# Performance work log

Measured on AMD Instinct MI355X. Metric: run time of the kernel, lower is better.

## Reference

```python
import jax, jax.numpy as jnp
import numpy as np

K = 3  # kernel_size=(3,3), flat all-ones structuring element


def _erode(x):
    # flat erosion = sliding-window min, SAME padding with +inf (geodesic)
    return jax.lax.reduce_window(x, float('inf'), jax.lax.min,
                                 (1, 1, K, K), (1, 1, 1, 1), 'SAME')


def _dilate(x):
    # flat dilation = sliding-window max, SAME padding with -inf
    return jax.lax.reduce_window(x, -float('inf'), jax.lax.max,
                                 (1, 1, K, K), (1, 1, 1, 1), 'SAME')


def setup_inputs() -> dict:
    key = jax.random.key(0)
    x = jax.random.uniform(key, (16, 3, 1024, 1024), dtype=jnp.float32)
    return {"x": x}


def reference(x) -> jnp.ndarray:
    # morphological opening: dilation(erosion(x)) with flat 3x3 SE,
    # applied per-channel (kernel repeated over channels in the original)
    return _dilate(_erode(x))
```

## Files before the change

kernel.cpp:

```cpp
#include <hip/hip_runtime.h>


#define IMG_H 1024
#define IMG_W 1024
#define TX 128
#define TY 16
#define IN_W (TX + 8)
#define IN_H (TY + 4)
#define ER_W (TX + 2)
#define ER_H (TY + 2)
#define NT 256

__global__ __launch_bounds__(NT)
void open3x3_fused(const float* __restrict__ in, float* __restrict__ out) {
    __shared__ float s_in[IN_H][IN_W];
    __shared__ float s_h [IN_H][ER_W];
    __shared__ float s_e [ER_H][ER_W];
    __shared__ float s_m [ER_H][TX];

    const int t  = threadIdx.x;
    const int ox = blockIdx.x * TX;
    const int oy = blockIdx.y * TY;
    const int img_elems = IMG_H * IMG_W;
    const float* img  = in  + (size_t)blockIdx.z * img_elems;
    float*       outp = out + (size_t)blockIdx.z * img_elems;

    const float PINF = __builtin_inff();
    const float NINF = -__builtin_inff();

    for (int idx = t; idx < IN_H * (IN_W / 4); idx += NT) {
        int row = idx / (IN_W / 4);
        int c4  = idx % (IN_W / 4);
        int r = oy - 2 + row;
        int c = ox - 4 + 4 * c4;
        float4 v;
        if (r >= 0 && r < IMG_H && c >= 0 && c + 3 < IMG_W) {
            v = *(const float4*)(img + r * IMG_W + c);
        } else {
            const float* rowp = img + r * IMG_W;
            bool rin = (r >= 0 && r < IMG_H);
            v.x = (rin && c + 0 >= 0 && c + 0 < IMG_W) ? rowp[c + 0] : PINF;
            v.y = (rin && c + 1 >= 0 && c + 1 < IMG_W) ? rowp[c + 1] : PINF;
            v.z = (rin && c + 2 >= 0 && c + 2 < IMG_W) ? rowp[c + 2] : PINF;
            v.w = (rin && c + 3 >= 0 && c + 3 < IMG_W) ? rowp[c + 3] : PINF;
        }
        *(float4*)&s_in[row][4 * c4] = v;
    }
    __syncthreads();

    for (int idx = t; idx < IN_H * ER_W; idx += NT) {
        int y = idx / ER_W;
        int x = idx % ER_W;
        int sx = x + 3;
        float a = s_in[y][sx - 1];
        float b = s_in[y][sx];
        float c = s_in[y][sx + 1];
        s_h[y][x] = fminf(fminf(a, b), c);
    }
    __syncthreads();

    for (int idx = t; idx < ER_H * ER_W; idx += NT) {
        int y = idx / ER_W;
        int x = idx % ER_W;
        int r = oy - 1 + y;
        int c = ox - 1 + x;
        float v;
        if (r < 0 || r >= IMG_H || c < 0 || c >= IMG_W) {
            v = NINF;
        } else {
            v = fminf(fminf(s_h[y][x], s_h[y + 1][x]), s_h[y + 2][x]);
        }
        s_e[y][x] = v;
    }
    __syncthreads();

    for (int idx = t; idx < ER_H * TX; idx += NT) {
        int y = idx / TX;
        int x = idx % TX;
        s_m[y][x] = fmaxf(fmaxf(s_e[y][x], s_e[y][x + 1]), s_e[y][x + 2]);
    }
    __syncthreads();

    for (int idx = t; idx < TY * (TX / 4); idx += NT) {
        int ty = idx / (TX / 4);
        int x4 = (idx % (TX / 4)) * 4;
        float4 v;
        v.x = fmaxf(fmaxf(s_m[ty][x4 + 0], s_m[ty + 1][x4 + 0]), s_m[ty + 2][x4 + 0]);
        v.y = fmaxf(fmaxf(s_m[ty][x4 + 1], s_m[ty + 1][x4 + 1]), s_m[ty + 2][x4 + 1]);
        v.z = fmaxf(fmaxf(s_m[ty][x4 + 2], s_m[ty + 1][x4 + 2]), s_m[ty + 2][x4 + 2]);
        v.w = fmaxf(fmaxf(s_m[ty][x4 + 3], s_m[ty + 1][x4 + 3]), s_m[ty + 2][x4 + 3]);
        *(float4*)(outp + (oy + ty) * IMG_W + ox + x4) = v;
    }
}

extern "C" void kernel_launch(void* const* d_in, const int* in_sizes, int n_in,
                              void* d_out, int out_size, void* d_ws, size_t ws_size,
                              hipStream_t stream) {
    const float* x = (const float*)d_in[0];
    float* out = (float*)d_out;
    dim3 grid(IMG_W / TX, IMG_H / TY, 48);
    dim3 block(NT);
    open3x3_fused<<<grid, block, 0, stream>>>(x, out);
}
```

Baseline: 381.1 us.

## Replace shared-memory staged opening with register rolling-window row sweep

Swaps the tiled shared-memory kernel, which had four staging passes and barriers, for a register-only kernel. Each block covers a full 1024-wide row strip, each thread owns 4 columns plus a 2-column halo, and the thread sweeps 32 rows while keeping horizontal-min and horizontal-max results in rolling registers. This removes shared-memory traffic, barriers and the redundant halo rows loaded per tile, at the cost of extra scalar halo loads and fewer blocks (1536). The next row is prefetched into registers to overlap its load with compute.

```diff
diff --git a/kernel.cpp b/kernel.cpp
--- a/kernel.cpp
+++ b/kernel.cpp
@@ -1,95 +1,103 @@
 #include <hip/hip_runtime.h>
 
 
-#define IMG_H 1024
-#define IMG_W 1024
-#define TX 128
-#define TY 16
-#define IN_W (TX + 8)
-#define IN_H (TY + 4)
-#define ER_W (TX + 2)
-#define ER_H (TY + 2)
+#define W 1024
+#define H 1024
+#define ROWS 32
 #define NT 256
 
 __global__ __launch_bounds__(NT)
-void open3x3_fused(const float* __restrict__ in, float* __restrict__ out) {
-    __shared__ float s_in[IN_H][IN_W];
-    __shared__ float s_h [IN_H][ER_W];
-    __shared__ float s_e [ER_H][ER_W];
-    __shared__ float s_m [ER_H][TX];
-
+void open3x3_reg(const float* __restrict__ in, float* __restrict__ out) {
     const int t  = threadIdx.x;
-    const int ox = blockIdx.x * TX;
-    const int oy = blockIdx.y * TY;
-    const int img_elems = IMG_H * IMG_W;
-    const float* img  = in  + (size_t)blockIdx.z * img_elems;
-    float*       outp = out + (size_t)blockIdx.z * img_elems;
+    const int c0 = 4 * t;
+    const int y0 = blockIdx.y * ROWS;
+    const size_t imgoff = (size_t)blockIdx.z * (size_t)(W * H);
+    const float* img  = in  + imgoff;
+    float*       outp = out + imgoff;
 
     const float PINF = __builtin_inff();
     const float NINF = -__builtin_inff();
 
-    for (int idx = t; idx < IN_H * (IN_W / 4); idx += NT) {
-        int row = idx / (IN_W / 4);
-        int c4  = idx % (IN_W / 4);
-        int r = oy - 2 + row;
-        int c = ox - 4 + 4 * c4;
-        float4 v;
-        if (r >= 0 && r < IMG_H && c >= 0 && c + 3 < IMG_W) {
-            v = *(const float4*)(img + r * IMG_W + c);
+    const bool has_l = (t > 0);
+    const bool has_r = (t < NT-1);
+
+    auto load_row = [&](int r, float x[8]) {
+        if (r >= 0 && r < H) {
+            const float* p = img + r * W;
+            float4 m = *(const float4*)(p + c0);
+            x[2] = m.x; x[3] = m.y; x[4] = m.z; x[5] = m.w;
+            x[0] = has_l ? p[c0 - 2] : PINF;
+            x[1] = has_l ? p[c0 - 1] : PINF;
+            x[6] = has_r ? p[c0 + 4] : PINF;
+            x[7] = has_r ? p[c0 + 5] : PINF;
         } else {
-            const float* rowp = img + r * IMG_W;
-            bool rin = (r >= 0 && r < IMG_H);
-            v.x = (rin && c + 0 >= 0 && c + 0 < IMG_W) ? rowp[c + 0] : PINF;
-            v.y = (rin && c + 1 >= 0 && c + 1 < IMG_W) ? rowp[c + 1] : PINF;
-            v.z = (rin && c + 2 >= 0 && c + 2 < IMG_W) ? rowp[c + 2] : PINF;
-            v.w = (rin && c + 3 >= 0 && c + 3 < IMG_W) ? rowp[c + 3] : PINF;
+            #pragma unroll
+            for (int i = 0; i < 8; i++) x[i] = PINF;
         }
-        *(float4*)&s_in[row][4 * c4] = v;
-    }
-    __syncthreads();
+    };
+    auto hmin6 = [&](const float x[8], float hm[6]) {
+        #pragma unroll
+        for (int i = 0; i < 6; i++) hm[i] = fminf(fminf(x[i], x[i+1]), x[i+2]);
+    };
+    auto erow = [&](int r, const float a[6], const float b[6], const float c[6],
+                    float e[6]) {
+        if (r >= 0 && r < H) {
+            #pragma unroll
+            for (int i = 0; i < 6; i++) e[i] = fminf(fminf(a[i], b[i]), c[i]);
+            if (!has_l) e[0] = NINF;
+            if (!has_r) e[5] = NINF;
+        } else {
+            #pragma unroll
+            for (int i = 0; i < 6; i++) e[i] = NINF;
+        }
+    };
+    auto hmax4 = [&](const float e[6], float hx[4]) {
+        #pragma unroll
+        for (int i = 0; i < 4; i++) hx[i] = fmaxf(fmaxf(e[i], e[i+1]), e[i+2]);
+    };
 
-    for (int idx = t; idx < IN_H * ER_W; idx += NT) {
-        int y = idx / ER_W;
-        int x = idx % ER_W;
-        int sx = x + 3;
-        float a = s_in[y][sx - 1];
-        float b = s_in[y][sx];
-        float c = s_in[y][sx + 1];
-        s_h[y][x] = fminf(fminf(a, b), c);
-    }
-    __syncthreads();
+    float x[8];
+    float hmP[6], hmQ[6], hmR[6], e[6];
+    float hx0[4], hx1[4], hx2[4];
 
-    for (int idx = t; idx < ER_H * ER_W; idx += NT) {
-        int y = idx / ER_W;
-        int x = idx % ER_W;
-        int r = oy - 1 + y;
-        int c = ox - 1 + x;
-        float v;
-        if (r < 0 || r >= IMG_H || c < 0 || c >= IMG_W) {
-            v = NINF;
-        } else {
-            v = fminf(fminf(s_h[y][x], s_h[y + 1][x]), s_h[y + 2][x]);
-        }
-        s_e[y][x] = v;
-    }
-    __syncthreads();
+    load_row(y0 - 2, x); hmin6(x, hmP);
+    load_row(y0 - 1, x); hmin6(x, hmQ);
+    load_row(y0,     x); hmin6(x, hmR);
+    erow(y0 - 1, hmP, hmQ, hmR, e); hmax4(e, hx0);
 
-    for (int idx = t; idx < ER_H * TX; idx += NT) {
-        int y = idx / TX;
-        int x = idx % TX;
-        s_m[y][x] = fmaxf(fmaxf(s_e[y][x], s_e[y][x + 1]), s_e[y][x + 2]);
-    }
-    __syncthreads();
+    #pragma unroll
+    for (int i = 0; i < 6; i++) { hmP[i] = hmQ[i]; hmQ[i] = hmR[i]; }
+    load_row(y0 + 1, x); hmin6(x, hmR);
+    erow(y0, hmP, hmQ, hmR, e); hmax4(e, hx1);
+    #pragma unroll
+    for (int i = 0; i < 6; i++) { hmP[i] = hmQ[i]; hmQ[i] = hmR[i]; }
 
-    for (int idx = t; idx < TY * (TX / 4); idx += NT) {
-        int ty = idx / (TX / 4);
-        int x4 = (idx % (TX / 4)) * 4;
-        float4 v;
-        v.x = fmaxf(fmaxf(s_m[ty][x4 + 0], s_m[ty + 1][x4 + 0]), s_m[ty + 2][x4 + 0]);
-        v.y = fmaxf(fmaxf(s_m[ty][x4 + 1], s_m[ty + 1][x4 + 1]), s_m[ty + 2][x4 + 1]);
-        v.z = fmaxf(fmaxf(s_m[ty][x4 + 2], s_m[ty + 1][x4 + 2]), s_m[ty + 2][x4 + 2]);
-        v.w = fmaxf(fmaxf(s_m[ty][x4 + 3], s_m[ty + 1][x4 + 3]), s_m[ty + 2][x4 + 3]);
-        *(float4*)(outp + (oy + ty) * IMG_W + ox + x4) = v;
+    float xc[8];
+    load_row(y0 + 2, xc);
+
+    #pragma unroll 4
+    for (int k = 0; k < ROWS; k++) {
+        const int y = y0 + k;
+        float xn[8];
+        if (k + 1 < ROWS) load_row(y + 3, xn);
+
+        hmin6(xc, hmR);
+        erow(y + 1, hmP, hmQ, hmR, e);
+        hmax4(e, hx2);
+
+        float4 o;
+        o.x = fmaxf(fmaxf(hx0[0], hx1[0]), hx2[0]);
+        o.y = fmaxf(fmaxf(hx0[1], hx1[1]), hx2[1]);
+        o.z = fmaxf(fmaxf(hx0[2], hx1[2]), hx2[2]);
+        o.w = fmaxf(fmaxf(hx0[3], hx1[3]), hx2[3]);
+        *(float4*)(outp + (size_t)y * W + c0) = o;
+
+        #pragma unroll
+        for (int i = 0; i < 4; i++) { hx0[i] = hx1[i]; hx1[i] = hx2[i]; }
+        #pragma unroll
+        for (int i = 0; i < 6; i++) { hmP[i] = hmQ[i]; hmQ[i] = hmR[i]; }
+        #pragma unroll
+        for (int i = 0; i < 8; i++) xc[i] = xn[i];
     }
 }
 
@@ -98,7 +106,7 @@
                               hipStream_t stream) {
     const float* x = (const float*)d_in[0];
     float* out = (float*)d_out;
-    dim3 grid(IMG_W / TX, IMG_H / TY, 48);
+    dim3 grid(1, H / ROWS, 48);
     dim3 block(NT);
-    open3x3_fused<<<grid, block, 0, stream>>>(x, out);
+    open3x3_reg<<<grid, block, 0, stream>>>(x, out);
 }
```

Measured after the change: 353.3 us. -7.3%, faster.
